# Performance work log

Measured on AMD Instinct MI355X. Metric: run time of the kernel, lower is better.

## Reference

```python
import jax, jax.numpy as jnp
import numpy as np

N_FEATURES = 16
NUM_LAYERS = 8
HIDDEN = 256
NUM_BINS = 8
RANGE_MIN, RANGE_MAX = -5.0, 5.0
MIN_BIN = 1e-4      # distrax RationalQuadraticSpline min_bin_size
MIN_SLOPE = 1e-4    # distrax min_knot_slope
LOC_ALPHA = 1.0
BATCH = 131072


def setup_inputs() -> dict:
    key = jax.random.key(0)
    ks = jax.random.split(key, 8)
    L, F, H = NUM_LAYERS, N_FEATURES, HIDDEN
    P = F * (3 * NUM_BINS + 1)  # 400
    x = jax.random.normal(ks[0], (BATCH, F), dtype=jnp.float32)
    # first Dense: variance_scaling(0.01,'fan_in','normal')
    W0 = (jax.random.normal(ks[1], (L, F, H)) * np.sqrt(0.01 / F)).astype(jnp.float32)
    b0 = jnp.zeros((L, H), jnp.float32)
    # residual-block denses (lecun-normal scale)
    Wr = (jax.random.normal(ks[2], (L, 4, H, H)) / np.sqrt(H)).astype(jnp.float32)
    br = jnp.zeros((L, 4, H), jnp.float32)
    # final Dense is zero-init in the module; use small random values so the
    # spline branch actually computes non-identity math for kernel testing.
    Wf = (jax.random.normal(ks[3], (L, H, P)) * 0.01).astype(jnp.float32)
    bf = (jax.random.normal(ks[4], (L, P)) * 0.01).astype(jnp.float32)
    scales = (1.0 + 0.05 * jax.random.normal(ks[5], (L, F))).astype(jnp.float32)
    shifts = (0.05 * jax.random.normal(ks[6], (L, F))).astype(jnp.float32)
    rng = np.random.RandomState(0)
    perms = jnp.array(np.stack([rng.permutation(F) for _ in range(L)]).astype(np.int32))
    return dict(x=x, W0=W0, b0=b0, Wr=Wr, br=br, Wf=Wf, bf=bf,
                scales=scales, shifts=shifts, perms=perms)


def _pe_mask(dtype):
    # sin_pe_func(pe_op='add', pe_t=1.0, pe_alpha=loc_alpha, pe_ratio=1.0)
    idx = jnp.arange(HIDDEN, dtype=dtype) / HIDDEN
    return LOC_ALPHA * jnp.sin(2.0 * jnp.pi * idx)


def _conditioner(xm, W0, b0, Wr, br, Wf, bf, pe):
    h = xm @ W0 + b0                                  # (B,H)
    for blk in range(2):
        y = h
        for j in range(2):
            y = jax.nn.relu(y + pe) @ Wr[2 * blk + j] + br[2 * blk + j]
        h = h + y
    h = jax.nn.relu(h)
    p = h @ Wf + bf                                   # (B, F*25)
    return p.reshape(p.shape[0], N_FEATURES, 3 * NUM_BINS + 1)


def _rqs_forward(x, params):
    # distrax RationalQuadraticSpline.forward_and_log_det, vectorized over (B,F)
    K = NUM_BINS
    uw, uh, us = params[..., :K], params[..., K:2 * K], params[..., 2 * K:]
    total = RANGE_MAX - RANGE_MIN
    w = jax.nn.softmax(uw, axis=-1) * (total - K * MIN_BIN) + MIN_BIN
    h = jax.nn.softmax(uh, axis=-1) * (total - K * MIN_BIN) + MIN_BIN
    offset = float(np.log(np.expm1(1.0 - MIN_SLOPE)))
    d = jax.nn.softplus(us + offset) + MIN_SLOPE       # (B,F,K+1) knot slopes
    zeros = jnp.zeros(x.shape + (1,), x.dtype)
    xk = RANGE_MIN + jnp.concatenate([zeros, jnp.cumsum(w, -1)], -1)  # (B,F,K+1)
    yk = RANGE_MIN + jnp.concatenate([zeros, jnp.cumsum(h, -1)], -1)
    idx = jnp.clip(jnp.sum((x[..., None] >= xk).astype(jnp.int32), -1) - 1, 0, K - 1)
    g = lambda a, i: jnp.take_along_axis(a, i[..., None], axis=-1)[..., 0]
    x0, x1 = g(xk, idx), g(xk, idx + 1)
    y0, y1 = g(yk, idx), g(yk, idx + 1)
    d0, d1 = g(d, idx), g(d, idx + 1)
    s = (y1 - y0) / (x1 - x0)
    z = jnp.clip((x - x0) / (x1 - x0), 0.0, 1.0)
    z1m = 1.0 - z
    den = s + (d1 + d0 - 2.0 * s) * z * z1m
    y_in = y0 + (y1 - y0) * (s * z * z + d0 * z * z1m) / den
    ld_in = (2.0 * jnp.log(s)
             + jnp.log(d1 * z * z + 2.0 * s * z * z1m + d0 * z1m * z1m)
             - 2.0 * jnp.log(den))
    inside = (x >= RANGE_MIN) & (x <= RANGE_MAX)      # identity outside range
    return jnp.where(inside, y_in, x), jnp.where(inside, ld_in, 0.0)


def _flow_log_prob(x, W0, b0, Wr, br, Wf, bf, scales, shifts, perms):
    B, F = x.shape
    pe = _pe_mask(x.dtype)
    mask = (jnp.arange(F) % 2).astype(bool)  # True = pass-through dim
    logdet = jnp.zeros((B,), x.dtype)
    for i in range(NUM_LAYERS):
        x = x[:, perms[i]]                                   # Permute (logdet 0)
        x = x * scales[i] + shifts[i]                        # all-dims ScalarAffine
        logdet = logdet + jnp.sum(jnp.log(jnp.abs(scales[i])))
        xm = jnp.where(mask, x, jnp.zeros_like(x))           # conditioner sees masked x
        params = _conditioner(xm, W0[i], b0[i], Wr[i], br[i], Wf[i], bf[i], pe)
        y, ld = _rqs_forward(x, params)                      # masked RQS coupling
        x = jnp.where(mask, x, y)
        logdet = logdet + jnp.sum(jnp.where(mask, jnp.zeros_like(ld), ld), axis=-1)
        mask = ~mask
    base_lp = -0.5 * jnp.sum(x * x, axis=-1) - 0.5 * F * jnp.log(2.0 * jnp.pi)
    return base_lp + logdet


def reference(x, W0, b0, Wr, br, Wf, bf, scales, shifts, perms):
    return _flow_log_prob(x, W0, b0, Wr, br, Wf, bf, scales, shifts, perms)
```

## Files before the change

### kernel.cpp

```cpp
#include <hip/hip_runtime.h>

#define NBATCH   131072
#define FDIM     16
#define NLAYER   8
#define HDIM     256
#define PCOLS    208
#define PSTRIDE  208
#define TSTRIDE  264
#define MTILE    128
#define NTHREADS 512

typedef unsigned short u16;
typedef __attribute__((ext_vector_type(8))) __bf16 bf16x8;
typedef __attribute__((ext_vector_type(8))) u16    u16x8;
typedef __attribute__((ext_vector_type(4))) u16    u16x4;
typedef __attribute__((ext_vector_type(2))) u16    u16x2;
typedef __attribute__((ext_vector_type(4))) float  f32x4;

#define WRP_OFF  0u
#define W0P_OFF  4194304u
#define WFP_OFF  4325376u
#define BFP_OFF  5177344u

__device__ __forceinline__ u16 f2bf(float f){
  __bf16 h = (__bf16)f;
  return __builtin_bit_cast(u16, h);
}
__device__ __forceinline__ float bf2f(u16 b){
  unsigned u = ((unsigned)b) << 16;
  return __builtin_bit_cast(float, u);
}
__device__ __forceinline__ f32x4 mfma16(bf16x8 a, bf16x8 b, f32x4 c){
  return __builtin_amdgcn_mfma_f32_16x16x32_bf16(a, b, c, 0, 0, 0);
}

__global__ void pack_wr_k(const float* __restrict__ Wr, u16* __restrict__ Wrp){
  int idx = blockIdx.x*256 + threadIdx.x;
  int n = idx & 255, g = (idx>>8)&3, ks = (idx>>10)&7, m = (idx>>13)&3, l = idx>>15;
  const float* src = Wr + (((size_t)(l*4+m)*HDIM + (ks*32+g*8))*HDIM + n);
  u16x8 v;
  #pragma unroll
  for (int j=0;j<8;++j) v[j] = f2bf(src[(size_t)j*HDIM]);
  *(u16x8*)(Wrp + (size_t)idx*8) = v;
}
__global__ void pack_w0_k(const float* __restrict__ W0, u16* __restrict__ W0p){
  int idx = blockIdx.x*256 + threadIdx.x;
  int n = idx&255, g=(idx>>8)&3, l=idx>>10;
  u16x8 v;
  #pragma unroll
  for (int j=0;j<8;++j){ int k=g*8+j; v[j] = (k<FDIM) ? f2bf(W0[(l*FDIM+k)*HDIM+n]) : (u16)0; }
  *(u16x8*)(W0p + (size_t)idx*8) = v;
}
__global__ void pack_wf_k(const float* __restrict__ Wf, u16* __restrict__ Wfp){
  int idx = blockIdx.x*256 + threadIdx.x;
  int nc = idx % PCOLS; int t = idx / PCOLS;
  int g = t&3, ks=(t>>2)&7, l=t>>5;
  int fs = nc/26, kk = nc%26;
  u16x8 v = {0,0,0,0,0,0,0,0};
  if (kk < 25){
    int f = 2*fs + (l&1);
    int col = f*25 + kk;
    #pragma unroll
    for (int j=0;j<8;++j){ int k=ks*32+g*8+j; v[j]=f2bf(Wf[((size_t)l*HDIM+k)*400+col]); }
  }
  *(u16x8*)(Wfp + (size_t)idx*8) = v;
}
__global__ void pack_bf_k(const float* __restrict__ bf, const float* __restrict__ scales,
                          float* __restrict__ bfp){
  int idx = blockIdx.x*256 + threadIdx.x;
  if (idx >= NLAYER*PCOLS) return;
  if (idx == NLAYER*PCOLS-1){
    float s = 0.f;
    for (int i=0;i<NLAYER*FDIM;++i) s += __logf(fabsf(scales[i]));
    bfp[idx] = s;
    return;
  }
  int nc = idx % PCOLS, l = idx / PCOLS;
  int fs = nc/26, kk = nc%26;
  float v = 0.f;
  if (kk < 25){ int f=2*fs+(l&1); v = bf[l*400 + f*25 + kk]; }
  bfp[idx] = v;
}

__global__ __launch_bounds__(NTHREADS, 2)
void flow_kernel(const float* __restrict__ xg,
                 const float* __restrict__ b0g,
                 const float* __restrict__ brg,
                 const float* __restrict__ scg,
                 const float* __restrict__ shg,
                 const int*   __restrict__ pmg,
                 const u16*   __restrict__ w0p,
                 const u16*   __restrict__ wrp,
                 const u16*   __restrict__ wfp,
                 const float* __restrict__ bfp,
                 float* __restrict__ outg)
{
  __shared__ u16   t_lds[MTILE*TSTRIDE];
  __shared__ float x_lds[MTILE*FDIM];
  __shared__ float pe_lds[HDIM];
  u16* p_lds = t_lds;

  const int tid  = threadIdx.x;
  const int wave = tid >> 6;
  const int lane = tid & 63;
  const int wm = wave >> 2;
  const int wn = wave & 3;
  const int lr = lane & 15;
  const int lg = lane >> 4;
  const int rowg0 = blockIdx.x * MTILE;
  const int srow = tid >> 2;
  const int sq   = tid & 3;

  if (tid < HDIM) pe_lds[tid] = sinf(6.283185307179586f * (float)tid / 256.0f);

  {
    float4 v = *(const float4*)(xg + (size_t)(rowg0+srow)*FDIM + sq*4);
    *(float4*)(x_lds + srow*FDIM + sq*4) = v;
  }
  float ld_acc = 0.f;
  __syncthreads();

  const bf16x8* wrp8 = (const bf16x8*)wrp;
  const bf16x8* w0p8 = (const bf16x8*)w0p;
  const bf16x8* wfp8 = (const bf16x8*)wfp;

  f32x4 h[16];

  auto stage_frags = [&](const f32x4* src, bool use_pe){
    #pragma unroll
    for (int mi=0; mi<4; ++mi){
      u16* dst = t_lds + (wm*64 + mi*16 + lr)*TSTRIDE;
      #pragma unroll
      for (int ni=0; ni<4; ++ni){
        const int col = wn*64 + ni*16 + lg*4;
        f32x4 v = src[mi*4+ni];
        if (use_pe){
          f32x4 pv = *(const f32x4*)(pe_lds + col);
          #pragma unroll
          for (int r=0;r<4;++r) v[r] += pv[r];
        }
        u16x4 pk;
        #pragma unroll
        for (int r=0;r<4;++r) pk[r] = f2bf(fmaxf(v[r], 0.f));
        *(u16x4*)(dst + col) = pk;
      }
    }
  };

  auto mm_hidden = [&](f32x4* acc, const bf16x8* wb8, const float* brp, bool accum){
    f32x4 res[16];
    #pragma unroll
    for (int ni=0; ni<4; ++ni){
      f32x4 bv = *(const f32x4*)(brp + wn*64 + ni*16 + lg*4);
      #pragma unroll
      for (int mi=0; mi<4; ++mi){
        f32x4 r0;
        #pragma unroll
        for (int r=0;r<4;++r) r0[r] = (accum ? acc[mi*4+ni][r] : 0.f) + bv[r];
        res[mi*4+ni] = r0;
      }
    }
    const int bofs  = lg*256 + wn*64 + lr;
    const int abase = (wm*64 + lr)*TSTRIDE;
    #pragma unroll
    for (int ks=0; ks<8; ++ks){
      bf16x8 w[4], a[4];
      #pragma unroll
      for (int ni=0; ni<4; ++ni)
        w[ni] = wb8[ks*1024 + bofs + ni*16];
      #pragma unroll
      for (int mi=0; mi<4; ++mi)
        a[mi] = *(const bf16x8*)(t_lds + abase + mi*16*TSTRIDE + ks*32 + lg*8);
      #pragma unroll
      for (int mi=0; mi<4; ++mi)
        #pragma unroll
        for (int ni=0; ni<4; ++ni)
          res[mi*4+ni] = mfma16(w[ni], a[mi], res[mi*4+ni]);
    }
    #pragma unroll
    for (int i=0;i<16;++i) acc[i] = res[i];
  };

  for (int li=0; li<NLAYER; ++li){
    {
      float tv[4];
      #pragma unroll
      for (int j=0;j<4;++j){
        const int f  = sq*4 + j;
        const int pf = pmg[li*FDIM + f];
        const float sc = scg[li*FDIM + f];
        tv[j] = x_lds[srow*FDIM + pf]*sc + shg[li*FDIM + f];
      }
      __syncthreads();
      #pragma unroll
      for (int j=0;j<4;++j) x_lds[srow*FDIM + sq*4 + j] = tv[j];
    }
    __syncthreads();

    {
      u16x8 pk;
      #pragma unroll
      for (int j=0;j<8;++j){
        const int f = sq*8 + j;
        float v = 0.f;
        if (f < FDIM && ((f & 1) != (li & 1))) v = x_lds[srow*FDIM + f];
        pk[j] = f2bf(v);
      }
      *(u16x8*)(t_lds + srow*TSTRIDE + sq*8) = pk;
    }
    __syncthreads();

    {
      bf16x8 w[4];
      #pragma unroll
      for (int ni=0; ni<4; ++ni)
        w[ni] = w0p8[li*1024 + lg*256 + wn*64 + ni*16 + lr];
      #pragma unroll
      for (int mi=0; mi<4; ++mi){
        bf16x8 a = *(const bf16x8*)(t_lds + (wm*64 + mi*16 + lr)*TSTRIDE + lg*8);
        #pragma unroll
        for (int ni=0; ni<4; ++ni){
          f32x4 z = {0.f,0.f,0.f,0.f};
          h[mi*4+ni] = mfma16(w[ni], a, z);
        }
      }
      #pragma unroll
      for (int ni=0; ni<4; ++ni){
        f32x4 bv = *(const f32x4*)(b0g + li*HDIM + wn*64 + ni*16 + lg*4);
        #pragma unroll
        for (int mi=0; mi<4; ++mi){
          #pragma unroll
          for (int r=0;r<4;++r) h[mi*4+ni][r] += bv[r];
        }
      }
    }
    __syncthreads();

    f32x4 y[16];
    #pragma unroll
    for (int blk=0; blk<2; ++blk){
      stage_frags(h, true);
      __syncthreads();
      mm_hidden(y, wrp8 + (size_t)(li*4 + 2*blk)*8192, brg + (li*4 + 2*blk)*HDIM, false);
      __syncthreads();
      stage_frags(y, true);
      __syncthreads();
      mm_hidden(h, wrp8 + (size_t)(li*4 + 2*blk+1)*8192, brg + (li*4 + 2*blk+1)*HDIM, true);
      __syncthreads();
    }

    stage_frags(h, false);
    __syncthreads();
    {
      const int NFRAG = (wn==0) ? 4 : 3;
      f32x4 pacc[16];
      #pragma unroll
      for (int i=0;i<16;++i){ f32x4 z={0.f,0.f,0.f,0.f}; pacc[i]=z; }
      const int abase = (wm*64 + lr)*TSTRIDE;
      #pragma unroll
      for (int ks=0; ks<8; ++ks){
        bf16x8 a[4];
        #pragma unroll
        for (int mi=0;mi<4;++mi)
          a[mi] = *(const bf16x8*)(t_lds + abase + mi*16*TSTRIDE + ks*32 + lg*8);
        #pragma unroll
        for (int t=0;t<4;++t){
          if (t < NFRAG){
            const int nf = wn + 4*t;
            bf16x8 w = wfp8[li*6656 + ks*832 + lg*208 + nf*16 + lr];
            #pragma unroll
            for (int mi=0;mi<4;++mi)
              pacc[mi*4+t] = mfma16(w, a[mi], pacc[mi*4+t]);
          }
        }
      }
      __syncthreads();
      #pragma unroll
      for (int t=0;t<4;++t){
        if (t < NFRAG){
          const int nf = wn + 4*t;
          const int col = nf*16 + lg*4;
          f32x4 bv = *(const f32x4*)(bfp + li*PCOLS + col);
          #pragma unroll
          for (int mi=0;mi<4;++mi){
            const int prow = wm*64 + mi*16 + lr;
            u16x4 pk;
            #pragma unroll
            for (int r=0;r<4;++r) pk[r] = f2bf(pacc[mi*4+t][r] + bv[r]);
            *(u16x4*)(p_lds + prow*PSTRIDE + col) = pk;
          }
        }
      }
    }
    __syncthreads();

    {
      #pragma unroll
      for (int e=0; e<2; ++e){
        const int fslot = sq*2 + e;
        const int ft = fslot*2 + (li & 1);
        const float xv = x_lds[srow*FDIM + ft];
        const u16* pp = p_lds + srow*PSTRIDE + fslot*26;
        float uw[8], uh[8], us[9];
        #pragma unroll
        for (int k2=0;k2<4;++k2){ u16x2 v = *(const u16x2*)(pp + 2*k2);      uw[2*k2]=bf2f(v[0]); uw[2*k2+1]=bf2f(v[1]); }
        #pragma unroll
        for (int k2=0;k2<4;++k2){ u16x2 v = *(const u16x2*)(pp + 8 + 2*k2);  uh[2*k2]=bf2f(v[0]); uh[2*k2+1]=bf2f(v[1]); }
        #pragma unroll
        for (int k2=0;k2<4;++k2){ u16x2 v = *(const u16x2*)(pp + 16 + 2*k2); us[2*k2]=bf2f(v[0]); us[2*k2+1]=bf2f(v[1]); }
        us[8] = bf2f(pp[24]);
        float mw = uw[0], mh = uh[0];
        #pragma unroll
        for (int k=1;k<8;++k){ mw=fmaxf(mw,uw[k]); mh=fmaxf(mh,uh[k]); }
        float sw=0.f, sh=0.f, bw[8], bh[8];
        #pragma unroll
        for (int k=0;k<8;++k){ bw[k]=__expf(uw[k]-mw); sw+=bw[k]; bh[k]=__expf(uh[k]-mh); sh+=bh[k]; }
        const float wscl = 9.9992f / sw;
        const float hscl = 9.9992f / sh;
        #pragma unroll
        for (int k=0;k<8;++k){ bw[k]=bw[k]*wscl + 1e-4f; bh[k]=bh[k]*hscl + 1e-4f; }
        float dv[9];
        #pragma unroll
        for (int k=0;k<9;++k){
          const float v = us[k] + 0.5411667f;
          const float spv = (v > 15.f) ? v : __logf(1.f + __expf(v));
          dv[k] = spv + 1e-4f;
        }
        const float xr = xv + 5.f;
        float cw=0.f, ch=0.f;
        float x0=0.f, y0=0.f, x1=0.f, y1=0.f, d0=0.f, d1=0.f;
        #pragma unroll
        for (int k=0;k<8;++k){
          const float nw = cw + bw[k];
          const float nh = ch + bh[k];
          const bool take = (k==0) || (xr >= cw);
          if (take){ x0=cw; y0=ch; x1=nw; y1=nh; d0=dv[k]; d1=dv[k+1]; }
          cw = nw; ch = nh;
        }
        const float dx = x1 - x0;
        const float s  = (y1 - y0) / dx;
        float z = (xr - x0) / dx;
        z = fminf(fmaxf(z, 0.f), 1.f);
        const float zm  = 1.f - z;
        const float den = s + (d1 + d0 - 2.f*s)*z*zm;
        const float yout = (y0 - 5.f) + (y1 - y0)*(s*z*z + d0*z*zm)/den;
        const float nrm  = d1*z*z + 2.f*s*z*zm + d0*zm*zm;
        const float ld   = __logf(s*s*nrm/(den*den));
        const bool inside = (xv >= -5.f) && (xv <= 5.f);
        x_lds[srow*FDIM + ft] = inside ? yout : xv;
        ld_acc += inside ? ld : 0.f;
      }
    }
    __syncthreads();
  }

  {
    float s2 = 0.f;
    #pragma unroll
    for (int j=0;j<4;++j){
      const float xv = x_lds[srow*FDIM + sq*4 + j];
      s2 += xv*xv;
    }
    float tot = ld_acc - 0.5f*s2;
    tot += __shfl_xor(tot, 1);
    tot += __shfl_xor(tot, 2);
    if (sq == 0){
      const float sumlogsc = bfp[NLAYER*PCOLS - 1];
      outg[rowg0 + srow] = tot + sumlogsc - 14.70301653127476f;
    }
  }
}

extern "C" void kernel_launch(void* const* d_in, const int* in_sizes, int n_in,
                              void* d_out, int out_size, void* d_ws, size_t ws_size,
                              hipStream_t stream) {
  (void)in_sizes; (void)n_in; (void)out_size; (void)ws_size;
  const float* x  = (const float*)d_in[0];
  const float* W0 = (const float*)d_in[1];
  const float* b0 = (const float*)d_in[2];
  const float* Wr = (const float*)d_in[3];
  const float* br = (const float*)d_in[4];
  const float* Wf = (const float*)d_in[5];
  const float* bf = (const float*)d_in[6];
  const float* sc = (const float*)d_in[7];
  const float* sh = (const float*)d_in[8];
  const int*   pm = (const int*)d_in[9];

  char* ws = (char*)d_ws;
  u16*   Wrp = (u16*)(ws + WRP_OFF);
  u16*   W0p = (u16*)(ws + W0P_OFF);
  u16*   Wfp = (u16*)(ws + WFP_OFF);
  float* bfp = (float*)(ws + BFP_OFF);

  pack_wr_k<<<1024, 256, 0, stream>>>(Wr, Wrp);
  pack_w0_k<<<32,   256, 0, stream>>>(W0, W0p);
  pack_wf_k<<<208,  256, 0, stream>>>(Wf, Wfp);
  pack_bf_k<<<7,    256, 0, stream>>>(bf, sc, bfp);

  flow_kernel<<<NBATCH/MTILE, NTHREADS, 0, stream>>>(
      x, b0, br, sc, sh, pm, W0p, Wrp, Wfp, bfp, (float*)d_out);
}
```

Before: 1.106 ms.

## Double-buffer LDS activation tile to drop block-wide barriers

Allocates two LDS activation buffers and alternates staging between them, so consecutive GEMM stages no longer need a barrier between reading one tile and writing the next. Several __syncthreads are removed, including the ones around the permutation and at the end of each layer, where only same-wave rows are touched. The P-tile stride is padded to reduce LDS bank conflicts. The trade-off is roughly double the LDS footprint per block, which may stop two 512-thread blocks from sharing a CU.

```diff
diff --git a/kernel.cpp b/kernel.cpp
--- a/kernel.cpp
+++ b/kernel.cpp
@@ -5,10 +5,11 @@
 #define NLAYER   8
 #define HDIM     256
 #define PCOLS    208
-#define PSTRIDE  208
+#define PSTRIDE  212
 #define TSTRIDE  264
 #define MTILE    128
 #define NTHREADS 512
+#define TBUF     (MTILE*TSTRIDE)
 
 typedef unsigned short u16;
 typedef __attribute__((ext_vector_type(8))) __bf16 bf16x8;
@@ -95,10 +96,9 @@
                  const float* __restrict__ bfp,
                  float* __restrict__ outg)
 {
-  __shared__ u16   t_lds[MTILE*TSTRIDE];
+  __shared__ u16   t_lds[2*TBUF];
   __shared__ float x_lds[MTILE*FDIM];
   __shared__ float pe_lds[HDIM];
-  u16* p_lds = t_lds;
 
   const int tid  = threadIdx.x;
   const int wave = tid >> 6;
@@ -126,10 +126,10 @@
 
   f32x4 h[16];
 
-  auto stage_frags = [&](const f32x4* src, bool use_pe){
+  auto stage_frags = [&](u16* tbase, const f32x4* src, bool use_pe){
     #pragma unroll
     for (int mi=0; mi<4; ++mi){
-      u16* dst = t_lds + (wm*64 + mi*16 + lr)*TSTRIDE;
+      u16* dst = tbase + (wm*64 + mi*16 + lr)*TSTRIDE;
       #pragma unroll
       for (int ni=0; ni<4; ++ni){
         const int col = wn*64 + ni*16 + lg*4;
@@ -147,7 +147,8 @@
     }
   };
 
-  auto mm_hidden = [&](f32x4* acc, const bf16x8* wb8, const float* brp, bool accum){
+  auto mm_hidden = [&](const u16* tbase, f32x4* acc, const bf16x8* wb8,
+                       const float* brp, bool accum){
     f32x4 res[16];
     #pragma unroll
     for (int ni=0; ni<4; ++ni){
@@ -170,7 +171,7 @@
         w[ni] = wb8[ks*1024 + bofs + ni*16];
       #pragma unroll
       for (int mi=0; mi<4; ++mi)
-        a[mi] = *(const bf16x8*)(t_lds + abase + mi*16*TSTRIDE + ks*32 + lg*8);
+        a[mi] = *(const bf16x8*)(tbase + abase + mi*16*TSTRIDE + ks*32 + lg*8);
       #pragma unroll
       for (int mi=0; mi<4; ++mi)
         #pragma unroll
@@ -181,7 +182,12 @@
     for (int i=0;i<16;++i) acc[i] = res[i];
   };
 
+  int tb = 0;
+
   for (int li=0; li<NLAYER; ++li){
+    u16* buf0 = t_lds + tb*TBUF;
+    u16* buf1 = t_lds + (tb^1)*TBUF;
+
     {
       float tv[4];
       #pragma unroll
@@ -191,11 +197,9 @@
         const float sc = scg[li*FDIM + f];
         tv[j] = x_lds[srow*FDIM + pf]*sc + shg[li*FDIM + f];
       }
-      __syncthreads();
       #pragma unroll
       for (int j=0;j<4;++j) x_lds[srow*FDIM + sq*4 + j] = tv[j];
     }
-    __syncthreads();
 
     {
       u16x8 pk;
@@ -206,7 +210,7 @@
         if (f < FDIM && ((f & 1) != (li & 1))) v = x_lds[srow*FDIM + f];
         pk[j] = f2bf(v);
       }
-      *(u16x8*)(t_lds + srow*TSTRIDE + sq*8) = pk;
+      *(u16x8*)(buf0 + srow*TSTRIDE + sq*8) = pk;
     }
     __syncthreads();
 
@@ -217,7 +221,7 @@
         w[ni] = w0p8[li*1024 + lg*256 + wn*64 + ni*16 + lr];
       #pragma unroll
       for (int mi=0; mi<4; ++mi){
-        bf16x8 a = *(const bf16x8*)(t_lds + (wm*64 + mi*16 + lr)*TSTRIDE + lg*8);
+        bf16x8 a = *(const bf16x8*)(buf0 + (wm*64 + mi*16 + lr)*TSTRIDE + lg*8);
         #pragma unroll
         for (int ni=0; ni<4; ++ni){
           f32x4 z = {0.f,0.f,0.f,0.f};
@@ -234,22 +238,22 @@
         }
       }
     }
-    __syncthreads();
 
     f32x4 y[16];
-    #pragma unroll
-    for (int blk=0; blk<2; ++blk){
-      stage_frags(h, true);
-      __syncthreads();
-      mm_hidden(y, wrp8 + (size_t)(li*4 + 2*blk)*8192, brg + (li*4 + 2*blk)*HDIM, false);
-      __syncthreads();
-      stage_frags(y, true);
-      __syncthreads();
-      mm_hidden(h, wrp8 + (size_t)(li*4 + 2*blk+1)*8192, brg + (li*4 + 2*blk+1)*HDIM, true);
-      __syncthreads();
-    }
-
-    stage_frags(h, false);
+    stage_frags(buf1, h, true);
+    __syncthreads();
+    mm_hidden(buf1, y, wrp8 + (size_t)(li*4 + 0)*8192, brg + (li*4 + 0)*HDIM, false);
+    stage_frags(buf0, y, true);
+    __syncthreads();
+    mm_hidden(buf0, h, wrp8 + (size_t)(li*4 + 1)*8192, brg + (li*4 + 1)*HDIM, true);
+    stage_frags(buf1, h, true);
+    __syncthreads();
+    mm_hidden(buf1, y, wrp8 + (size_t)(li*4 + 2)*8192, brg + (li*4 + 2)*HDIM, false);
+    stage_frags(buf0, y, true);
+    __syncthreads();
+    mm_hidden(buf0, h, wrp8 + (size_t)(li*4 + 3)*8192, brg + (li*4 + 3)*HDIM, true);
+
+    stage_frags(buf1, h, false);
     __syncthreads();
     {
       const int NFRAG = (wn==0) ? 4 : 3;
@@ -262,7 +266,7 @@
         bf16x8 a[4];
         #pragma unroll
         for (int mi=0;mi<4;++mi)
-          a[mi] = *(const bf16x8*)(t_lds + abase + mi*16*TSTRIDE + ks*32 + lg*8);
+          a[mi] = *(const bf16x8*)(buf1 + abase + mi*16*TSTRIDE + ks*32 + lg*8);
         #pragma unroll
         for (int t=0;t<4;++t){
           if (t < NFRAG){
@@ -274,7 +278,6 @@
           }
         }
       }
-      __syncthreads();
       #pragma unroll
       for (int t=0;t<4;++t){
         if (t < NFRAG){
@@ -287,7 +290,7 @@
             u16x4 pk;
             #pragma unroll
             for (int r=0;r<4;++r) pk[r] = f2bf(pacc[mi*4+t][r] + bv[r]);
-            *(u16x4*)(p_lds + prow*PSTRIDE + col) = pk;
+            *(u16x4*)(buf0 + prow*PSTRIDE + col) = pk;
           }
         }
       }
@@ -300,7 +303,7 @@
         const int fslot = sq*2 + e;
         const int ft = fslot*2 + (li & 1);
         const float xv = x_lds[srow*FDIM + ft];
-        const u16* pp = p_lds + srow*PSTRIDE + fslot*26;
+        const u16* pp = buf0 + srow*PSTRIDE + fslot*26;
         float uw[8], uh[8], us[9];
         #pragma unroll
         for (int k2=0;k2<4;++k2){ u16x2 v = *(const u16x2*)(pp + 2*k2);      uw[2*k2]=bf2f(v[0]); uw[2*k2+1]=bf2f(v[1]); }
@@ -351,7 +354,7 @@
         ld_acc += inside ? ld : 0.f;
       }
     }
-    __syncthreads();
+    tb ^= 1;
   }
 
   {
```

Result: faster. 1.055 ms (-4.6%).
